# Performance work log

Measured on AMD Instinct MI355X. Metric: run time of the kernel, lower is better.

The kernel has to match this reference:

```python
import jax, jax.numpy as jnp
import numpy as np

EMBED_DIM = 1024
ATTEN_DIM = 64


def setup_inputs() -> dict:
    key = jax.random.key(0)
    k_x, k_q, k_k, k_v = jax.random.split(key, 4)
    B, S = 4, 4096
    scale = 1.0 / np.sqrt(EMBED_DIM)
    x = jax.random.normal(k_x, (B, S, EMBED_DIM), dtype=jnp.float32)
    # torch nn.Linear weights are [out_features, in_features]
    Wq = jax.random.normal(k_q, (ATTEN_DIM, EMBED_DIM), dtype=jnp.float32) * scale
    Wk = jax.random.normal(k_k, (ATTEN_DIM, EMBED_DIM), dtype=jnp.float32) * scale
    Wv = jax.random.normal(k_v, (ATTEN_DIM, EMBED_DIM), dtype=jnp.float32) * scale
    return {"x": x, "Wq": Wq, "Wk": Wk, "Wv": Wv}


def reference(x, Wq, Wk, Wv):
    # q, k, v: [B, S, D]
    q = jnp.einsum('bse,de->bsd', x, Wq)
    k = jnp.einsum('bse,de->bsd', x, Wk)
    v = jnp.einsum('bse,de->bsd', x, Wv)
    d = k.shape[-1]
    scores = jnp.einsum('bsd,btd->bst', q, k) / jnp.sqrt(jnp.float32(d))
    S = x.shape[1]
    causal = jnp.tril(jnp.ones((S, S), dtype=bool))
    scores = jnp.where(causal[None, :, :], scores, -jnp.inf)
    attn = jax.nn.softmax(scores, axis=-1)
    return jnp.einsum('bst,btd->bsd', attn, v)
```

## Files before the change

kernel.cpp:

```cpp
#include <hip/hip_runtime.h>
#include <hip/hip_bf16.h>
#include <stdint.h>

typedef __attribute__((ext_vector_type(8))) short  short8;
typedef __attribute__((ext_vector_type(4))) short  short4v;
typedef __attribute__((ext_vector_type(4))) float  float4v;

#define MFMA16(a, b, c) __builtin_amdgcn_mfma_f32_16x16x32_bf16((a), (b), (c), 0, 0, 0)

#define S_LEN  4096
#define NBATCH 4
#define EMB    1024
#define DD     64
#define NROWS  (NBATCH * S_LEN)
#define SCL2   0.1803368801111204f

#define AS1 const __attribute__((address_space(1))) unsigned int*
#define AS3 __attribute__((address_space(3))) unsigned int*

static __device__ __forceinline__ short f2bf(float f) {
  uint32_t u = __float_as_uint(f);
  return (short)((u + 0x7FFFu + ((u >> 16) & 1u)) >> 16);
}
static __device__ __forceinline__ unsigned pk2(float a, float b) {
  union { __hip_bfloat162 h; unsigned u; } z;
  z.h = __float22bfloat162_rn(make_float2(a, b));
  return z.u;
}
static __device__ __forceinline__ short8 cvt8(float4v a, float4v b) {
  union { unsigned u[4]; short8 s; } z;
  z.u[0] = pk2(a[0], a[1]); z.u[1] = pk2(a[2], a[3]);
  z.u[2] = pk2(b[0], b[1]); z.u[3] = pk2(b[2], b[3]);
  return z.s;
}

__global__ void wcvt_kernel(const float* __restrict__ Wq, const float* __restrict__ Wk,
                            const float* __restrict__ Wv, short* __restrict__ Wb2) {
  const int t   = blockIdx.x * 256 + threadIdx.x;
  const int row = t >> 7;
  const int k   = (t & 127) * 8;
  const float* src = (row < 64) ? (Wq + (size_t)row * EMB)
                   : (row < 128) ? (Wk + (size_t)(row - 64) * EMB)
                                 : (Wv + (size_t)(row - 128) * EMB);
  const float sc = (row < 64) ? SCL2 : 1.0f;
  float4v a = *(const float4v*)(src + k);
  float4v b = *(const float4v*)(src + k + 4);
#pragma unroll
  for (int i = 0; i < 4; ++i) { a[i] *= sc; b[i] *= sc; }
  *(short8*)(Wb2 + (((k >> 5) * 192 + row) << 5) + (k & 31)) = cvt8(a, b);
}

__global__ __launch_bounds__(256, 2) void qkv_kernel(
    const float* __restrict__ x, const short* __restrict__ Wb2,
    short* __restrict__ Qb, short* __restrict__ Kb, short* __restrict__ Vt) {
  __shared__ float As[2][2048];
  __shared__ short Bs[2][12288];

  const int tid  = threadIdx.x;
  const int w    = tid >> 6;
  const int lane = tid & 63;
  const int ln   = lane & 15;
  const int quad = lane >> 4;
  const int m0   = blockIdx.x * 32;
  const int wr   = w & 1;
  const int wc   = w >> 1;

  const int tA0 = 2 * w, tA1 = 2 * w + 1;
  const float* xA0 = x + (size_t)(m0 + ((tA0 >> 2) << 4) + (lane >> 2)) * EMB
                       + ((tA0 & 3) * 4 + (lane & 3)) * 4;
  const float* xA1 = x + (size_t)(m0 + ((tA1 >> 2) << 4) + (lane >> 2)) * EMB
                       + ((tA1 & 3) * 4 + (lane & 3)) * 4;
  const short* wB = Wb2 + (size_t)(6 * w) * 512 + lane * 8;

#define STAGE(S, BUF) do {                                                      \
    __builtin_amdgcn_global_load_lds((AS1)(xA0 + (S) * 64),                     \
        (AS3)&As[BUF][tA0 * 256], 16, 0, 0);                                    \
    __builtin_amdgcn_global_load_lds((AS1)(xA1 + (S) * 64),                     \
        (AS3)&As[BUF][tA1 * 256], 16, 0, 0);                                    \
    _Pragma("unroll")                                                           \
    for (int j = 0; j < 6; ++j)                                                 \
      __builtin_amdgcn_global_load_lds((AS1)(wB + (size_t)(S) * 12288 + j * 512),\
          (AS3)&Bs[BUF][(6 * w + j) * 512], 16, 0, 0);                          \
  } while (0)

  const float4v zz = {0.f, 0.f, 0.f, 0.f};
  float4v acc[6] = {zz, zz, zz, zz, zz, zz};

  STAGE(0, 0);
  int buf = 0;
  for (int s = 0; s < 16; ++s) {
    __syncthreads();
    if (s + 1 < 16) STAGE(s + 1, buf ^ 1);
    short8 aF[2];
#pragma unroll
    for (int h = 0; h < 2; ++h) {
      const int ai = (wr * 4 + 2 * h + (quad >> 1)) * 256 + (ln * 4 + (quad & 1) * 2) * 4;
      const float4v lo = *(const float4v*)&As[buf][ai];
      const float4v hi = *(const float4v*)&As[buf][ai + 4];
      aF[h] = cvt8(lo, hi);
    }
#pragma unroll
    for (int f = 0; f < 6; ++f) {
      const int cf = wc * 6 + f;
      const short8 b0 = *(const short8*)&Bs[buf][(cf * 16 + ln) * 32 + quad * 8];
      const short8 b1 = *(const short8*)&Bs[buf][6144 + (cf * 16 + ln) * 32 + quad * 8];
      if (wc == 0 || f < 2) {
        acc[f] = MFMA16(aF[0], b0, acc[f]);
        acc[f] = MFMA16(aF[1], b1, acc[f]);
      } else {
        acc[f] = MFMA16(b0, aF[0], acc[f]);
        acc[f] = MFMA16(b1, aF[1], acc[f]);
      }
    }
    buf ^= 1;
  }
#undef STAGE

  const int b  = m0 >> 12;
  const int sb = m0 & (S_LEN - 1);
  if (wc == 0) {
#pragma unroll
    for (int f = 0; f < 6; ++f)
#pragma unroll
      for (int r = 0; r < 4; ++r) {
        const int row = m0 + wr * 16 + quad * 4 + r;
        if (f < 4) Qb[(size_t)row * DD + f * 16 + ln] = f2bf(acc[f][r]);
        else       Kb[(size_t)row * DD + (f - 4) * 16 + ln] = f2bf(acc[f][r]);
      }
  } else {
#pragma unroll
    for (int f = 0; f < 2; ++f)
#pragma unroll
      for (int r = 0; r < 4; ++r) {
        const int row = m0 + wr * 16 + quad * 4 + r;
        Kb[(size_t)row * DD + 32 + f * 16 + ln] = f2bf(acc[f][r]);
      }
#pragma unroll
    for (int f = 2; f < 6; ++f)
#pragma unroll
      for (int r = 0; r < 4; ++r) {
        const int d = (f - 2) * 16 + quad * 4 + r;
        Vt[((size_t)b * DD + d) * S_LEN + sb + wr * 16 + ln] = f2bf(acc[f][r]);
      }
  }
}

#define PSTRW 76

__global__ __launch_bounds__(512, 2) void attn_kernel(
    const short* __restrict__ Qb, const short* __restrict__ Kb,
    const short* __restrict__ Vt, float* __restrict__ out) {
  __shared__ float sbuf[8][32 * PSTRW];
  __shared__ float llds[8][32];

  const int tid  = threadIdx.x;
  const int w    = tid >> 6;
  const int lane = tid & 63;
  const int ln   = lane & 15;
  const int quad = lane >> 4;
  const int g    = blockIdx.x;
  const int b    = g & 3;
  const int j    = g >> 2;
  const short* Kbase = Kb + (size_t)b * S_LEN * DD;
  const short* Vbase = Vt + (size_t)b * DD * S_LEN;
  float* pw = &sbuf[w][0];
  const float4v zz = {0.f, 0.f, 0.f, 0.f};

  for (int ph = 0; ph < 2; ++ph) {
    const int band = ph ? (127 - j) : j;
    const int qb   = band * 32;
    const int qg0  = b * S_LEN + qb;

    short8 aQ[2][2];
#pragma unroll
    for (int rfi = 0; rfi < 2; ++rfi)
#pragma unroll
      for (int h = 0; h < 2; ++h)
        aQ[rfi][h] = *(const short8*)(Qb + (size_t)(qg0 + rfi * 16 + ln) * DD + h * 32 + quad * 8);

    float4v o[2][4];
    float lp[2][4];
#pragma unroll
    for (int rfi = 0; rfi < 2; ++rfi)
#pragma unroll
      for (int d = 0; d < 4; ++d) { o[rfi][d] = zz; lp[rfi][d] = 0.f; }

    const int T = (qb + 95) >> 6;

    short8 Kc[4][2], Kn[4][2];
#pragma unroll
    for (int c = 0; c < 4; ++c)
#pragma unroll
      for (int h = 0; h < 2; ++h)
        Kc[c][h] = *(const short8*)(Kbase + (size_t)(w * 64 + c * 16 + ln) * DD + h * 32 + quad * 8);

    for (int it = w; it < T; it += 8) {
      const int kv0 = it * 64;
      short8 Vc[4][2];
#pragma unroll
      for (int d = 0; d < 4; ++d)
#pragma unroll
        for (int h = 0; h < 2; ++h)
          Vc[d][h] = *(const short8*)(Vbase + (size_t)(d * 16 + ln) * S_LEN + kv0 + h * 32 + quad * 8);

      float4v s[2][4];
#pragma unroll
      for (int rfi = 0; rfi < 2; ++rfi)
#pragma unroll
        for (int c = 0; c < 4; ++c) {
          s[rfi][c] = MFMA16(aQ[rfi][0], Kc[c][0], zz);
          s[rfi][c] = MFMA16(aQ[rfi][1], Kc[c][1], s[rfi][c]);
        }

      const int kvn = (it + 8 < T) ? (it + 8) * 64 : 0;
#pragma unroll
      for (int c = 0; c < 4; ++c)
#pragma unroll
        for (int h = 0; h < 2; ++h)
          Kn[c][h] = *(const short8*)(Kbase + (size_t)(kvn + c * 16 + ln) * DD + h * 32 + quad * 8);

      const bool needmask = (kv0 + 63) > qb;
#pragma unroll
      for (int rfi = 0; rfi < 2; ++rfi) {
        float p[4][4];
#pragma unroll
        for (int c = 0; c < 4; ++c)
#pragma unroll
          for (int r = 0; r < 4; ++r) {
            float e = exp2f(fminf(s[rfi][c][r], 60.0f));
            if (needmask && (kv0 + c * 16 + ln > qb + rfi * 16 + quad * 4 + r)) e = 0.f;
            p[c][r] = e;
          }
#pragma unroll
        for (int r = 0; r < 4; ++r)
          lp[rfi][r] += p[0][r] + p[1][r] + p[2][r] + p[3][r];
#pragma unroll
        for (int c = 0; c < 4; ++c)
#pragma unroll
          for (int r = 0; r < 4; ++r)
            pw[(rfi * 16 + quad * 4 + r) * PSTRW + c * 16 + ln] = p[c][r];
      }
      asm volatile("s_waitcnt lgkmcnt(0)" ::: "memory");
      short8 aP[2][2];
#pragma unroll
      for (int rfi = 0; rfi < 2; ++rfi)
#pragma unroll
        for (int h = 0; h < 2; ++h) {
          const float4v lo = *(const float4v*)&pw[(rfi * 16 + ln) * PSTRW + h * 32 + quad * 8];
          const float4v hi = *(const float4v*)&pw[(rfi * 16 + ln) * PSTRW + h * 32 + quad * 8 + 4];
          aP[rfi][h] = cvt8(lo, hi);
        }
#pragma unroll
      for (int rfi = 0; rfi < 2; ++rfi)
#pragma unroll
        for (int d = 0; d < 4; ++d) {
          o[rfi][d] = MFMA16(aP[rfi][0], Vc[d][0], o[rfi][d]);
          o[rfi][d] = MFMA16(aP[rfi][1], Vc[d][1], o[rfi][d]);
        }
#pragma unroll
      for (int c = 0; c < 4; ++c)
#pragma unroll
        for (int h = 0; h < 2; ++h)
          Kc[c][h] = Kn[c][h];
    }

#pragma unroll
    for (int rfi = 0; rfi < 2; ++rfi)
#pragma unroll
      for (int r = 0; r < 4; ++r) {
        float lr = lp[rfi][r];
        lr += __shfl_xor(lr, 1);
        lr += __shfl_xor(lr, 2);
        lr += __shfl_xor(lr, 4);
        lr += __shfl_xor(lr, 8);
        if (ln == 0) llds[w][rfi * 16 + quad * 4 + r] = lr;
#pragma unroll
        for (int d = 0; d < 4; ++d)
          pw[(rfi * 16 + quad * 4 + r) * 64 + d * 16 + ln] = o[rfi][d][r];
      }
    __syncthreads();

#pragma unroll
    for (int jj = 0; jj < 4; ++jj) {
      const int idx = tid + jj * 512;
      const int row = idx >> 6, col = idx & 63;
      float sum = 0.f, lt = 0.f;
#pragma unroll
      for (int wi = 0; wi < 8; ++wi) {
        sum += sbuf[wi][row * 64 + col];
        lt  += llds[wi][row];
      }
      out[(size_t)(qg0 + row) * DD + col] = sum / lt;
    }
    __syncthreads();
  }
}

extern "C" void kernel_launch(void* const* d_in, const int* in_sizes, int n_in,
                              void* d_out, int out_size, void* d_ws, size_t ws_size,
                              hipStream_t stream) {
  const float* x  = (const float*)d_in[0];
  const float* Wq = (const float*)d_in[1];
  const float* Wk = (const float*)d_in[2];
  const float* Wv = (const float*)d_in[3];

  short* Qb  = (short*)d_ws;
  short* Kb  = Qb + (size_t)NROWS * DD;
  short* Vt  = Kb + (size_t)NROWS * DD;
  short* Wb2 = Vt + (size_t)NROWS * DD;

  wcvt_kernel<<<dim3(96), dim3(256), 0, stream>>>(Wq, Wk, Wv, Wb2);
  qkv_kernel<<<dim3(NROWS / 32), dim3(256), 0, stream>>>(x, Wb2, Qb, Kb, Vt);
  attn_kernel<<<dim3(NBATCH * 64), dim3(512), 0, stream>>>(Qb, Kb, Vt, (float*)d_out);
}
```

Baseline: 161.5 us.

## Restructure attention into 16-row bands with async global-to-LDS double-buffered K/V

The attention kernel now processes 16-query-row bands with 4 waves per block, launching twice as many blocks. Each wave stages its own K and V tiles into LDS with global_load_lds, double-buffered so the next tile's loads overlap the current tile's MFMAs. It also uses the hardware exp2 and reciprocal intrinsics. The goal is better occupancy and causal load balance plus hidden memory latency, at the cost of halving work per block and more LDS traffic per tile.

After: 181.5 us. 12.4% more time.

```diff
diff --git a/kernel.cpp b/kernel.cpp
--- a/kernel.cpp
+++ b/kernel.cpp
@@ -145,13 +145,12 @@
   }
 }
 
-#define PSTRW 76
-
-__global__ __launch_bounds__(512, 2) void attn_kernel(
+__global__ __launch_bounds__(256, 2) void attn_kernel(
     const short* __restrict__ Qb, const short* __restrict__ Kb,
     const short* __restrict__ Vt, float* __restrict__ out) {
-  __shared__ float sbuf[8][32 * PSTRW];
-  __shared__ float llds[8][32];
+  __shared__ short kvbuf[4][2][4096];
+  __shared__ float pbuf[4][16 * 36];
+  __shared__ float llds[4][16];
 
   const int tid  = threadIdx.x;
   const int w    = tid >> 6;
@@ -161,139 +160,137 @@
   const int g    = blockIdx.x;
   const int b    = g & 3;
   const int j    = g >> 2;
+
   const short* Kbase = Kb + (size_t)b * S_LEN * DD;
   const short* Vbase = Vt + (size_t)b * DD * S_LEN;
-  float* pw = &sbuf[w][0];
+  const int koff = (lane & 7) * DD + (lane >> 3) * 8;
+  const size_t voff = (size_t)(lane & 15) * S_LEN + (lane >> 4) * 8;
+  float* pw = &pbuf[w][0];
   const float4v zz = {0.f, 0.f, 0.f, 0.f};
 
+#define KVSTAGE(KV0, BUF) do {                                                  \
+    const short* kp_ = Kbase + (size_t)(KV0) * DD + koff;                       \
+    const short* vp_ = Vbase + (KV0) + voff;                                    \
+    _Pragma("unroll")                                                           \
+    for (int s5 = 0; s5 < 4; ++s5)                                              \
+      __builtin_amdgcn_global_load_lds((AS1)(kp_ + s5 * 8 * DD),                \
+          (AS3)&kvbuf[w][BUF][s5 * 512], 16, 0, 0);                             \
+    _Pragma("unroll")                                                           \
+    for (int s5 = 0; s5 < 4; ++s5)                                              \
+      __builtin_amdgcn_global_load_lds((AS1)(vp_ + (size_t)(s5 * 16) * S_LEN),  \
+          (AS3)&kvbuf[w][BUF][2048 + s5 * 512], 16, 0, 0);                      \
+  } while (0)
+
   for (int ph = 0; ph < 2; ++ph) {
-    const int band = ph ? (127 - j) : j;
-    const int qb   = band * 32;
+    const int band = ph ? (255 - j) : j;
+    const int qb   = band * 16;
     const int qg0  = b * S_LEN + qb;
-
-    short8 aQ[2][2];
-#pragma unroll
-    for (int rfi = 0; rfi < 2; ++rfi)
-#pragma unroll
-      for (int h = 0; h < 2; ++h)
-        aQ[rfi][h] = *(const short8*)(Qb + (size_t)(qg0 + rfi * 16 + ln) * DD + h * 32 + quad * 8);
-
-    float4v o[2][4];
-    float lp[2][4];
-#pragma unroll
-    for (int rfi = 0; rfi < 2; ++rfi)
-#pragma unroll
-      for (int d = 0; d < 4; ++d) { o[rfi][d] = zz; lp[rfi][d] = 0.f; }
-
-    const int T = (qb + 95) >> 6;
-
-    short8 Kc[4][2], Kn[4][2];
-#pragma unroll
-    for (int c = 0; c < 4; ++c)
-#pragma unroll
-      for (int h = 0; h < 2; ++h)
-        Kc[c][h] = *(const short8*)(Kbase + (size_t)(w * 64 + c * 16 + ln) * DD + h * 32 + quad * 8);
-
-    for (int it = w; it < T; it += 8) {
-      const int kv0 = it * 64;
-      short8 Vc[4][2];
-#pragma unroll
-      for (int d = 0; d < 4; ++d)
-#pragma unroll
-        for (int h = 0; h < 2; ++h)
-          Vc[d][h] = *(const short8*)(Vbase + (size_t)(d * 16 + ln) * S_LEN + kv0 + h * 32 + quad * 8);
-
-      float4v s[2][4];
-#pragma unroll
-      for (int rfi = 0; rfi < 2; ++rfi)
-#pragma unroll
-        for (int c = 0; c < 4; ++c) {
-          s[rfi][c] = MFMA16(aQ[rfi][0], Kc[c][0], zz);
-          s[rfi][c] = MFMA16(aQ[rfi][1], Kc[c][1], s[rfi][c]);
+    const int T    = (qb + 47) >> 5;
+
+    short8 aQ[2];
+#pragma unroll
+    for (int h = 0; h < 2; ++h)
+      aQ[h] = *(const short8*)(Qb + (size_t)(qg0 + ln) * DD + h * 32 + quad * 8);
+
+    float4v o[4] = {zz, zz, zz, zz};
+    float lp[4]  = {0.f, 0.f, 0.f, 0.f};
+
+    if (w < T) KVSTAGE(w * 32, 0);
+    int buf = 0;
+
+    for (int it = w; it < T; it += 4) {
+      const int kv0 = it * 32;
+      if (it + 4 < T) {
+        KVSTAGE((it + 4) * 32, buf ^ 1);
+        asm volatile("s_waitcnt vmcnt(8)" ::: "memory");
+      } else {
+        asm volatile("s_waitcnt vmcnt(0)" ::: "memory");
+      }
+      const short* kb_ = &kvbuf[w][buf][0];
+      const short* vb_ = &kvbuf[w][buf][2048];
+
+      float4v s[2] = {zz, zz};
+#pragma unroll
+      for (int ct = 0; ct < 2; ++ct)
+#pragma unroll
+        for (int h = 0; h < 2; ++h) {
+          const short8 kf = *(const short8*)(kb_ + (ct * 2 + (ln >> 3)) * 512
+                                                 + (ln & 7) * 8 + (h * 4 + quad) * 64);
+          s[ct] = MFMA16(aQ[h], kf, s[ct]);
         }
 
-      const int kvn = (it + 8 < T) ? (it + 8) * 64 : 0;
-#pragma unroll
-      for (int c = 0; c < 4; ++c)
-#pragma unroll
-        for (int h = 0; h < 2; ++h)
-          Kn[c][h] = *(const short8*)(Kbase + (size_t)(kvn + c * 16 + ln) * DD + h * 32 + quad * 8);
-
-      const bool needmask = (kv0 + 63) > qb;
-#pragma unroll
-      for (int rfi = 0; rfi < 2; ++rfi) {
-        float p[4][4];
-#pragma unroll
-        for (int c = 0; c < 4; ++c)
+      short8 vf[4];
+#pragma unroll
+      for (int dt = 0; dt < 4; ++dt)
+        vf[dt] = *(const short8*)(vb_ + dt * 512 + ln * 8 + quad * 128);
+
+      if (kv0 + 31 > qb) {
+#pragma unroll
+        for (int ct = 0; ct < 2; ++ct)
 #pragma unroll
           for (int r = 0; r < 4; ++r) {
-            float e = exp2f(fminf(s[rfi][c][r], 60.0f));
-            if (needmask && (kv0 + c * 16 + ln > qb + rfi * 16 + quad * 4 + r)) e = 0.f;
-            p[c][r] = e;
+            float e = __builtin_amdgcn_exp2f(fminf(s[ct][r], 60.0f));
+            if (kv0 + ct * 16 + ln > qb + quad * 4 + r) e = 0.f;
+            s[ct][r] = e;
           }
+      } else {
+#pragma unroll
+        for (int ct = 0; ct < 2; ++ct)
+#pragma unroll
+          for (int r = 0; r < 4; ++r)
+            s[ct][r] = __builtin_amdgcn_exp2f(fminf(s[ct][r], 60.0f));
+      }
+#pragma unroll
+      for (int r = 0; r < 4; ++r) lp[r] += s[0][r] + s[1][r];
+
+#pragma unroll
+      for (int ct = 0; ct < 2; ++ct)
 #pragma unroll
         for (int r = 0; r < 4; ++r)
-          lp[rfi][r] += p[0][r] + p[1][r] + p[2][r] + p[3][r];
-#pragma unroll
-        for (int c = 0; c < 4; ++c)
-#pragma unroll
-          for (int r = 0; r < 4; ++r)
-            pw[(rfi * 16 + quad * 4 + r) * PSTRW + c * 16 + ln] = p[c][r];
-      }
+          pw[(quad * 4 + r) * 36 + ct * 16 + ln] = s[ct][r];
       asm volatile("s_waitcnt lgkmcnt(0)" ::: "memory");
-      short8 aP[2][2];
-#pragma unroll
-      for (int rfi = 0; rfi < 2; ++rfi)
-#pragma unroll
-        for (int h = 0; h < 2; ++h) {
-          const float4v lo = *(const float4v*)&pw[(rfi * 16 + ln) * PSTRW + h * 32 + quad * 8];
-          const float4v hi = *(const float4v*)&pw[(rfi * 16 + ln) * PSTRW + h * 32 + quad * 8 + 4];
-          aP[rfi][h] = cvt8(lo, hi);
-        }
-#pragma unroll
-      for (int rfi = 0; rfi < 2; ++rfi)
-#pragma unroll
-        for (int d = 0; d < 4; ++d) {
-          o[rfi][d] = MFMA16(aP[rfi][0], Vc[d][0], o[rfi][d]);
-          o[rfi][d] = MFMA16(aP[rfi][1], Vc[d][1], o[rfi][d]);
-        }
-#pragma unroll
-      for (int c = 0; c < 4; ++c)
-#pragma unroll
-        for (int h = 0; h < 2; ++h)
-          Kc[c][h] = Kn[c][h];
-    }
-
-#pragma unroll
-    for (int rfi = 0; rfi < 2; ++rfi)
-#pragma unroll
-      for (int r = 0; r < 4; ++r) {
-        float lr = lp[rfi][r];
-        lr += __shfl_xor(lr, 1);
-        lr += __shfl_xor(lr, 2);
-        lr += __shfl_xor(lr, 4);
-        lr += __shfl_xor(lr, 8);
-        if (ln == 0) llds[w][rfi * 16 + quad * 4 + r] = lr;
-#pragma unroll
-        for (int d = 0; d < 4; ++d)
-          pw[(rfi * 16 + quad * 4 + r) * 64 + d * 16 + ln] = o[rfi][d][r];
-      }
+      const float4v lo = *(const float4v*)&pw[ln * 36 + quad * 8];
+      const float4v hi = *(const float4v*)&pw[ln * 36 + quad * 8 + 4];
+      const short8 aP = cvt8(lo, hi);
+#pragma unroll
+      for (int dt = 0; dt < 4; ++dt)
+        o[dt] = MFMA16(aP, vf[dt], o[dt]);
+
+      buf ^= 1;
+    }
+
+#pragma unroll
+    for (int r = 0; r < 4; ++r) {
+      float lr = lp[r];
+      lr += __shfl_xor(lr, 1);
+      lr += __shfl_xor(lr, 2);
+      lr += __shfl_xor(lr, 4);
+      lr += __shfl_xor(lr, 8);
+      if (ln == 0) llds[w][quad * 4 + r] = lr;
+    }
+    float* ow = (float*)&kvbuf[w][0][0];
+#pragma unroll
+    for (int dt = 0; dt < 4; ++dt)
+#pragma unroll
+      for (int r = 0; r < 4; ++r)
+        ow[(quad * 4 + r) * 64 + dt * 16 + ln] = o[dt][r];
     __syncthreads();
 
 #pragma unroll
     for (int jj = 0; jj < 4; ++jj) {
-      const int idx = tid + jj * 512;
+      const int idx = tid + jj * 256;
       const int row = idx >> 6, col = idx & 63;
       float sum = 0.f, lt = 0.f;
 #pragma unroll
-      for (int wi = 0; wi < 8; ++wi) {
-        sum += sbuf[wi][row * 64 + col];
+      for (int wi = 0; wi < 4; ++wi) {
+        sum += ((const float*)&kvbuf[wi][0][0])[row * 64 + col];
         lt  += llds[wi][row];
       }
-      out[(size_t)(qg0 + row) * DD + col] = sum / lt;
+      out[(size_t)(qg0 + row) * DD + col] = sum * __builtin_amdgcn_rcpf(lt);
     }
     __syncthreads();
   }
+#undef KVSTAGE
 }
 
 extern "C" void kernel_launch(void* const* d_in, const int* in_sizes, int n_in,
@@ -311,5 +308,5 @@
 
   wcvt_kernel<<<dim3(96), dim3(256), 0, stream>>>(Wq, Wk, Wv, Wb2);
   qkv_kernel<<<dim3(NROWS / 32), dim3(256), 0, stream>>>(x, Wb2, Qb, Kb, Vt);
-  attn_kernel<<<dim3(NBATCH * 64), dim3(512), 0, stream>>>(Qb, Kb, Vt, (float*)d_out);
-}
+  attn_kernel<<<dim3(NBATCH * 128), dim3(256), 0, stream>>>(Qb, Kb, Vt, (float*)d_out);
+}
```
